# Performance work log

Measured on AMD Instinct MI355X. Metric: run time of the kernel, lower is better.

The kernel has to match this reference:

```python
import jax, jax.numpy as jnp
import numpy as np

N = 65536      # nodes
E = 1048576    # edges (avg in-degree ~16)
C = 128        # in_channels = out_channels = edge_dim
T = 4          # towers
F_IN = C // T  # 32 (divide_input=True)
F_OUT = C // T # 32

# degree histogram from the repo: degrees 1..6 with these counts
_counts = np.array([108477, 299931, 180702, 10767, 3, 2], dtype=np.float64)
_degs = np.arange(1, 7, dtype=np.float64)
AVG_LIN = float((_counts * _degs).sum() / _counts.sum())
AVG_LOG = float((_counts * np.log(_degs + 1.0)).sum() / _counts.sum())


def setup_inputs() -> dict:
    key = jax.random.key(0)
    ks = jax.random.split(key, 8)
    def w(k, shape, fan_in):
        return (jax.random.normal(k, shape, jnp.float32) / np.sqrt(fan_in)).astype(jnp.float32)
    return {
        "x": jax.random.normal(ks[0], (N, C), jnp.float32),
        "edge_attr": jax.random.normal(ks[1], (E, C), jnp.float32),
        "edge_index": jax.random.randint(ks[2], (2, E), 0, N, jnp.int32),
        "W_edge": w(ks[3], (F_IN, C), C),
        "b_edge": jnp.zeros((F_IN,), jnp.float32),
        "W_pre": w(ks[4], (T, 3 * F_IN, F_IN), 3 * F_IN),
        "b_pre": jnp.zeros((T, F_IN), jnp.float32),
        "W_post": w(ks[5], (T, 13 * F_IN, F_OUT), 13 * F_IN),
        "b_post": jnp.zeros((T, F_OUT), jnp.float32),
        "W_lin": w(ks[6], (C, C), C),
        "b_lin": jnp.zeros((C,), jnp.float32),
    }


def reference(x, edge_attr, edge_index, W_edge, b_edge, W_pre, b_pre, W_post, b_post, W_lin, b_lin):
    src, dst = edge_index[0], edge_index[1]  # PyG: messages from src (x_j) aggregated at dst (x_i)
    xt = x.reshape(N, T, F_IN)               # divide_input=True: split channels across towers

    # edge encoder, broadcast across towers
    e = edge_attr @ W_edge.T + b_edge        # [E, F_in]
    e = jnp.broadcast_to(e[:, None, :], (E, T, F_IN))

    # message: gather + concat + per-tower pretrans Linear
    h = jnp.concatenate([xt[dst], xt[src], e], axis=-1)      # [E, T, 3F]
    m = jnp.einsum('etf,tfg->etg', h, W_pre) + b_pre          # [E, T, F]

    # multi-aggregator scatter-reduce over destination nodes
    cnt = jax.ops.segment_sum(jnp.ones((E,), m.dtype), dst, N)    # in-degree [N]
    cnt_safe = jnp.maximum(cnt, 1.0)[:, None, None]
    msum = jax.ops.segment_sum(m, dst, N)
    mean = msum / cnt_safe
    mean_sq = jax.ops.segment_sum(m * m, dst, N) / cnt_safe
    std = jnp.sqrt(jax.nn.relu(mean_sq - mean * mean) + 1e-5)
    empty = (cnt == 0)[:, None, None]
    mx = jnp.where(empty, 0.0, jax.ops.segment_max(m, dst, N))
    mn = jnp.where(empty, 0.0, jax.ops.segment_min(m, dst, N))
    agg = jnp.concatenate([mean, mx, mn, std], axis=-1)       # [N, T, 4F]

    # degree scalers: identity, amplification, attenuation
    deg = cnt[:, None, None]
    logd = jnp.log(deg + 1.0)
    amp = agg * (logd / AVG_LOG)
    att = agg * jnp.where(deg == 0, 1.0, AVG_LOG / jnp.where(deg == 0, 1.0, logd))
    out = jnp.concatenate([agg, amp, att], axis=-1)           # [N, T, 12F]

    # posttrans: concat self features, per-tower Linear, merge towers
    out = jnp.concatenate([xt, out], axis=-1)                 # [N, T, 13F]
    out = jnp.einsum('ntf,tfg->ntg', out, W_post) + b_post    # [N, T, F_out]
    out = out.reshape(N, C)
    return out @ W_lin.T + b_lin + x  # residual
```

## Files before the change

kernel.cpp:

```cpp
#include <hip/hip_runtime.h>
#include <math.h>

__global__ __launch_bounds__(256) void pre_kernel(
    const float* __restrict__ x, const float* __restrict__ W_pre,
    float* __restrict__ ps)
{
  __shared__ float xl[2][128];
  const int tid = threadIdx.x;
  const int nl  = tid >> 7;
  const int j   = tid & 127;
  const int n   = blockIdx.x * 2 + nl;
  xl[nl][j] = x[(size_t)n * 128 + j];
  __syncthreads();
  const int t = j >> 5, g = j & 31;
  const float* xp = &xl[nl][t * 32];
  const float* Ws = W_pre + (size_t)(t * 96 + 32) * 32 + g;
  float aps = 0.f;
#pragma unroll
  for (int f = 0; f < 32; ++f) aps += xp[f] * Ws[f * 32];
  ps[(size_t)n * 128 + j] = aps;
}

__global__ __launch_bounds__(256) void count_kernel(
    const int* __restrict__ ei, int* __restrict__ cnt, int E)
{
  const int e = blockIdx.x * 256 + threadIdx.x;
  if (e < E) atomicAdd(&cnt[ei[E + e]], 1);
}

__global__ __launch_bounds__(256) void scan_kernel(
    const int* __restrict__ cnt, int* __restrict__ base, int* __restrict__ fill)
{
  __shared__ int part[256];
  const int tid = threadIdx.x;
  const int c0 = tid * 256;
  int s = 0;
  for (int i = 0; i < 256; ++i) s += cnt[c0 + i];
  part[tid] = s;
  __syncthreads();
  if (tid == 0) {
    int run = 0;
    for (int i = 0; i < 256; ++i) { int t = part[i]; part[i] = run; run += t; }
  }
  __syncthreads();
  int run = part[tid];
  for (int i = 0; i < 256; ++i) {
    int cc = cnt[c0 + i];
    base[c0 + i] = run;
    fill[c0 + i] = run;
    run += cc;
  }
}

__global__ __launch_bounds__(256) void scatter_kernel(
    const int* __restrict__ ei, int* __restrict__ fill,
    int* __restrict__ eid_s, int* __restrict__ srcs_s, int E)
{
  const int e = blockIdx.x * 256 + threadIdx.x;
  if (e < E) {
    const int d = ei[E + e];
    const int slot = atomicAdd(&fill[d], 1);
    eid_s[slot] = e;
    srcs_s[slot] = ei[e];
  }
}

__global__ __launch_bounds__(256) void agg_kernel(
    const float* __restrict__ x, const float* __restrict__ edge_attr,
    const float* __restrict__ W_edge, const float* __restrict__ b_edge,
    const float* __restrict__ W_pre, const float* __restrict__ b_pre,
    const float* __restrict__ ps, const int* __restrict__ eid_s,
    const int* __restrict__ srcs_s, const int* __restrict__ cnt,
    const int* __restrict__ base, float* __restrict__ aggs)
{
  __shared__ float sEA[4][128];
  __shared__ float sE[4][32];
  __shared__ float sX[4][128];
  const int tid  = threadIdx.x;
  const int lane = tid & 63;
  const int w    = tid >> 6;
  const int g    = lane & 31;
  const int half = lane >> 5;
  const int t0   = half;
  const int n    = blockIdx.x * 4 + w;

  float we[64];
  {
    const float4* wrow = (const float4*)(W_edge + (size_t)g * 128 + half * 64);
#pragma unroll
    for (int k = 0; k < 16; ++k) {
      const float4 q = wrow[k];
      we[4*k] = q.x; we[4*k+1] = q.y; we[4*k+2] = q.z; we[4*k+3] = q.w;
    }
  }
  float wp0[32], wp1[32];
#pragma unroll
  for (int f = 0; f < 32; ++f) {
    wp0[f] = W_pre[(size_t)(t0 * 96 + 64 + f) * 32 + g];
    wp1[f] = W_pre[(size_t)((t0 + 2) * 96 + 64 + f) * 32 + g];
  }
  const float bedge = b_edge[g];

  sX[w][lane]      = x[(size_t)n * 128 + lane];
  sX[w][lane + 64] = x[(size_t)n * 128 + 64 + lane];
  float pd0 = b_pre[t0 * 32 + g];
  float pd1 = b_pre[(t0 + 2) * 32 + g];
#pragma unroll
  for (int f = 0; f < 32; ++f) {
    pd0 += sX[w][t0 * 32 + f]       * W_pre[(size_t)(t0 * 96 + f) * 32 + g];
    pd1 += sX[w][(t0 + 2) * 32 + f] * W_pre[(size_t)((t0 + 2) * 96 + f) * 32 + g];
  }

  const int c  = cnt[n];
  const int b0 = base[n];
  float sum0 = 0.f, sum1 = 0.f, sq0 = 0.f, sq1 = 0.f;
  float mx0 = -INFINITY, mx1 = -INFINITY, mn0 = INFINITY, mn1 = INFINITY;
  for (int i = 0; i < c; ++i) {
    const int idx = b0 + i;
    const int eid = eid_s[idx];
    const int s   = srcs_s[idx];
    const float2 v = *(const float2*)(edge_attr + (size_t)eid * 128 + lane * 2);
    *(float2*)&sEA[w][lane * 2] = v;
    const float ps0 = ps[(size_t)s * 128 + lane];
    const float ps1 = ps[(size_t)s * 128 + 64 + lane];
    float acc = 0.f;
    const float4* eap = (const float4*)&sEA[w][half * 64];
#pragma unroll
    for (int k = 0; k < 16; ++k) {
      const float4 q = eap[k];
      acc += q.x * we[4*k] + q.y * we[4*k+1] + q.z * we[4*k+2] + q.w * we[4*k+3];
    }
    acc += __shfl_xor(acc, 32);
    sE[w][g] = acc + bedge;
    float a0 = 0.f, a1 = 0.f;
    const float4* ep = (const float4*)sE[w];
#pragma unroll
    for (int k = 0; k < 8; ++k) {
      const float4 q = ep[k];
      a0 += q.x * wp0[4*k] + q.y * wp0[4*k+1] + q.z * wp0[4*k+2] + q.w * wp0[4*k+3];
      a1 += q.x * wp1[4*k] + q.y * wp1[4*k+1] + q.z * wp1[4*k+2] + q.w * wp1[4*k+3];
    }
    const float m0 = a0 + pd0 + ps0;
    const float m1 = a1 + pd1 + ps1;
    sum0 += m0; sq0 += m0 * m0; mx0 = fmaxf(mx0, m0); mn0 = fminf(mn0, m0);
    sum1 += m1; sq1 += m1 * m1; mx1 = fmaxf(mx1, m1); mn1 = fminf(mn1, m1);
  }

  const float csafe = fmaxf((float)c, 1.f);
  const float mean0 = sum0 / csafe, mean1 = sum1 / csafe;
  const float sd0 = sqrtf(fmaxf(sq0 / csafe - mean0 * mean0, 0.f) + 1e-5f);
  const float sd1 = sqrtf(fmaxf(sq1 / csafe - mean1 * mean1, 0.f) + 1e-5f);
  if (c == 0) { mx0 = mx1 = mn0 = mn1 = 0.f; }
  float* ag = aggs + (size_t)n * 512;
  ag[lane]       = mean0; ag[64 + lane]  = mean1;
  ag[128 + lane] = mx0;   ag[192 + lane] = mx1;
  ag[256 + lane] = mn0;   ag[320 + lane] = mn1;
  ag[384 + lane] = sd0;   ag[448 + lane] = sd1;
}

__global__ __launch_bounds__(256) void post_kernel(
    const float* __restrict__ x, const float* __restrict__ aggs,
    const int* __restrict__ cnt,
    const float* __restrict__ W_post, const float* __restrict__ b_post,
    const float* __restrict__ W_lin, const float* __restrict__ b_lin,
    float* __restrict__ out, float avg_log)
{
  __shared__ float vec[8][4][416];
  __shared__ float h2[8][128];
  const int tid = threadIdx.x;
  const int j = tid & 127;
  const int t = j >> 5, g = j & 31;
  const int n0 = blockIdx.x * 8;

  for (int itn = 0; itn < 4; ++itn) {
    const int nl = itn * 2 + (tid >> 7);
    const int n = n0 + nl;
    const size_t o = (size_t)n * 128 + j;
    const float* ag = aggs + (size_t)n * 512;
    const float c = (float)cnt[n];
    const float mean = ag[j];
    const float mx   = ag[128 + j];
    const float mn   = ag[256 + j];
    const float sd   = ag[384 + j];
    const float logd = logf(c + 1.f);
    const float amp_s = logd / avg_log;
    const float att_s = (c == 0.f) ? 1.f : (avg_log / logd);
    float* v = vec[nl][t];
    v[g]        = x[o];
    v[32 + g]   = mean;          v[64 + g]   = mx;
    v[96 + g]   = mn;            v[128 + g]  = sd;
    v[160 + g]  = mean * amp_s;  v[192 + g]  = mx * amp_s;
    v[224 + g]  = mn * amp_s;    v[256 + g]  = sd * amp_s;
    v[288 + g]  = mean * att_s;  v[320 + g]  = mx * att_s;
    v[352 + g]  = mn * att_s;    v[384 + g]  = sd * att_s;
  }
  __syncthreads();

  {
    const int nlb = tid >> 7;
    const float b = b_post[t * 32 + g];
    float acc0 = b, acc1 = b, acc2 = b, acc3 = b;
    const float* Wp = W_post + (size_t)(t * 416) * 32 + g;
    const float* v0 = vec[nlb + 0][t];
    const float* v1 = vec[nlb + 2][t];
    const float* v2 = vec[nlb + 4][t];
    const float* v3 = vec[nlb + 6][t];
    for (int f = 0; f < 416; ++f) {
      const float wv = Wp[(size_t)f * 32];
      acc0 += v0[f] * wv; acc1 += v1[f] * wv;
      acc2 += v2[f] * wv; acc3 += v3[f] * wv;
    }
    h2[nlb + 0][j] = acc0; h2[nlb + 2][j] = acc1;
    h2[nlb + 4][j] = acc2; h2[nlb + 6][j] = acc3;
  }
  __syncthreads();

  {
    const int nlb = tid >> 7;
    const float* Wl = W_lin + (size_t)j * 128;
    const float bl = b_lin[j];
    float a0 = bl, a1 = bl, a2 = bl, a3 = bl;
    const float* h0 = h2[nlb + 0];
    const float* h1 = h2[nlb + 2];
    const float* hp = h2[nlb + 4];
    const float* h3 = h2[nlb + 6];
    for (int k = 0; k < 128; ++k) {
      const float wv = Wl[k];
      a0 += h0[k] * wv; a1 += h1[k] * wv;
      a2 += hp[k] * wv; a3 += h3[k] * wv;
    }
    const size_t b0 = (size_t)(n0 + nlb + 0) * 128 + j;
    const size_t b1 = (size_t)(n0 + nlb + 2) * 128 + j;
    const size_t b2 = (size_t)(n0 + nlb + 4) * 128 + j;
    const size_t b3 = (size_t)(n0 + nlb + 6) * 128 + j;
    out[b0] = a0 + x[b0];
    out[b1] = a1 + x[b1];
    out[b2] = a2 + x[b2];
    out[b3] = a3 + x[b3];
  }
}

extern "C" void kernel_launch(void* const* d_in, const int* in_sizes, int n_in,
                              void* d_out, int out_size, void* d_ws, size_t ws_size,
                              hipStream_t stream) {
  const float* x         = (const float*)d_in[0];
  const float* edge_attr = (const float*)d_in[1];
  const int*   ei        = (const int*)  d_in[2];
  const float* W_edge    = (const float*)d_in[3];
  const float* b_edge    = (const float*)d_in[4];
  const float* W_pre     = (const float*)d_in[5];
  const float* b_pre     = (const float*)d_in[6];
  const float* W_post    = (const float*)d_in[7];
  const float* b_post    = (const float*)d_in[8];
  const float* W_lin     = (const float*)d_in[9];
  const float* b_lin     = (const float*)d_in[10];
  float* out = (float*)d_out;

  const int N = in_sizes[0] / 128;
  const int E = in_sizes[2] / 2;

  float* ps    = (float*)d_ws;
  float* aggs  = ps + (size_t)N * 128;
  int*   eid_s = (int*)(aggs + (size_t)N * 512);
  int*   srcs_s = eid_s + E;
  int*   cnt   = srcs_s + E;
  int*   base  = cnt + N;
  int*   fill  = base + N;

  hipMemsetAsync(cnt, 0, (size_t)N * 4, stream);

  const double counts[6] = {108477.0, 299931.0, 180702.0, 10767.0, 3.0, 2.0};
  double num = 0.0, den = 0.0;
  for (int i = 0; i < 6; ++i) { num += counts[i] * log((double)(i + 2)); den += counts[i]; }
  const float avg_log = (float)(num / den);

  pre_kernel<<<N / 2, 256, 0, stream>>>(x, W_pre, ps);
  count_kernel<<<(E + 255) / 256, 256, 0, stream>>>(ei, cnt, E);
  scan_kernel<<<1, 256, 0, stream>>>(cnt, base, fill);
  scatter_kernel<<<(E + 255) / 256, 256, 0, stream>>>(ei, fill, eid_s, srcs_s, E);
  agg_kernel<<<N / 4, 256, 0, stream>>>(x, edge_attr, W_edge, b_edge, W_pre, b_pre,
                                        ps, eid_s, srcs_s, cnt, base, aggs);
  post_kernel<<<N / 8, 256, 0, stream>>>(x, aggs, cnt, W_post, b_post,
                                         W_lin, b_lin, out, avg_log);
}
```

Measured before the change: 2.018 ms.

## Move edge encoder into scatter pass and prefetch sorted edge features in aggregation

```diff
diff --git a/kernel.cpp b/kernel.cpp
--- a/kernel.cpp
+++ b/kernel.cpp
@@ -52,29 +52,74 @@
   }
 }
 
-__global__ __launch_bounds__(256) void scatter_kernel(
-    const int* __restrict__ ei, int* __restrict__ fill,
-    int* __restrict__ eid_s, int* __restrict__ srcs_s, int E)
-{
-  const int e = blockIdx.x * 256 + threadIdx.x;
-  if (e < E) {
+__global__ __launch_bounds__(256) void escatter_kernel(
+    const float* __restrict__ edge_attr, const int* __restrict__ ei,
+    const float* __restrict__ W_edge, const float* __restrict__ b_edge,
+    int* __restrict__ fill, int* __restrict__ srcs_s,
+    float* __restrict__ e_sorted, int E)
+{
+  __shared__ float sEA[4][2][128];
+  const int tid  = threadIdx.x;
+  const int lane = tid & 63;
+  const int w    = tid >> 6;
+  const int g    = lane & 31;
+  const int half = lane >> 5;
+  const int e4   = (blockIdx.x * 4 + w) * 4;
+  if (e4 >= E) return;
+  const int nv = min(4, E - e4);
+
+  float we[64];
+  {
+    const float4* wrow = (const float4*)(W_edge + (size_t)g * 128 + half * 64);
+#pragma unroll
+    for (int k = 0; k < 16; ++k) {
+      const float4 q = wrow[k];
+      we[4*k] = q.x; we[4*k+1] = q.y; we[4*k+2] = q.z; we[4*k+3] = q.w;
+    }
+  }
+  const float bedge = b_edge[g];
+
+  int slot = 0;
+  if (lane < nv) {
+    const int e = e4 + lane;
     const int d = ei[E + e];
-    const int slot = atomicAdd(&fill[d], 1);
-    eid_s[slot] = e;
-    srcs_s[slot] = ei[e];
+    const int s = ei[e];
+    slot = atomicAdd(&fill[d], 1);
+    srcs_s[slot] = s;
+  }
+
+  float2 va[4];
+#pragma unroll
+  for (int l = 0; l < 4; ++l) {
+    const int el = (l < nv) ? (e4 + l) : e4;
+    va[l] = *(const float2*)(edge_attr + (size_t)el * 128 + lane * 2);
+  }
+
+#pragma unroll
+  for (int l = 0; l < 4; ++l) {
+    if (l >= nv) break;
+    *(float2*)&sEA[w][l & 1][lane * 2] = va[l];
+    float acc = 0.f;
+    const float4* eap = (const float4*)&sEA[w][l & 1][half * 64];
+#pragma unroll
+    for (int k = 0; k < 16; ++k) {
+      const float4 q = eap[k];
+      acc += q.x * we[4*k] + q.y * we[4*k+1] + q.z * we[4*k+2] + q.w * we[4*k+3];
+    }
+    acc += __shfl_xor(acc, 32);
+    const int sl = __shfl(slot, l);
+    if (half == 0) e_sorted[(size_t)sl * 32 + g] = acc + bedge;
   }
 }
 
 __global__ __launch_bounds__(256) void agg_kernel(
-    const float* __restrict__ x, const float* __restrict__ edge_attr,
-    const float* __restrict__ W_edge, const float* __restrict__ b_edge,
+    const float* __restrict__ x,
     const float* __restrict__ W_pre, const float* __restrict__ b_pre,
-    const float* __restrict__ ps, const int* __restrict__ eid_s,
+    const float* __restrict__ ps, const float* __restrict__ e_sorted,
     const int* __restrict__ srcs_s, const int* __restrict__ cnt,
     const int* __restrict__ base, float* __restrict__ aggs)
 {
-  __shared__ float sEA[4][128];
-  __shared__ float sE[4][32];
+  __shared__ float sE[4][2][64];
   __shared__ float sX[4][128];
   const int tid  = threadIdx.x;
   const int lane = tid & 63;
@@ -84,22 +129,12 @@
   const int t0   = half;
   const int n    = blockIdx.x * 4 + w;
 
-  float we[64];
-  {
-    const float4* wrow = (const float4*)(W_edge + (size_t)g * 128 + half * 64);
-#pragma unroll
-    for (int k = 0; k < 16; ++k) {
-      const float4 q = wrow[k];
-      we[4*k] = q.x; we[4*k+1] = q.y; we[4*k+2] = q.z; we[4*k+3] = q.w;
-    }
-  }
   float wp0[32], wp1[32];
 #pragma unroll
   for (int f = 0; f < 32; ++f) {
     wp0[f] = W_pre[(size_t)(t0 * 96 + 64 + f) * 32 + g];
     wp1[f] = W_pre[(size_t)((t0 + 2) * 96 + 64 + f) * 32 + g];
   }
-  const float bedge = b_edge[g];
 
   sX[w][lane]      = x[(size_t)n * 128 + lane];
   sX[w][lane + 64] = x[(size_t)n * 128 + 64 + lane];
@@ -115,35 +150,61 @@
   const int b0 = base[n];
   float sum0 = 0.f, sum1 = 0.f, sq0 = 0.f, sq1 = 0.f;
   float mx0 = -INFINITY, mx1 = -INFINITY, mn0 = INFINITY, mn1 = INFINITY;
-  for (int i = 0; i < c; ++i) {
-    const int idx = b0 + i;
-    const int eid = eid_s[idx];
-    const int s   = srcs_s[idx];
-    const float2 v = *(const float2*)(edge_attr + (size_t)eid * 128 + lane * 2);
-    *(float2*)&sEA[w][lane * 2] = v;
-    const float ps0 = ps[(size_t)s * 128 + lane];
-    const float ps1 = ps[(size_t)s * 128 + 64 + lane];
-    float acc = 0.f;
-    const float4* eap = (const float4*)&sEA[w][half * 64];
-#pragma unroll
-    for (int k = 0; k < 16; ++k) {
-      const float4 q = eap[k];
-      acc += q.x * we[4*k] + q.y * we[4*k+1] + q.z * we[4*k+2] + q.w * we[4*k+3];
-    }
-    acc += __shfl_xor(acc, 32);
-    sE[w][g] = acc + bedge;
-    float a0 = 0.f, a1 = 0.f;
-    const float4* ep = (const float4*)sE[w];
-#pragma unroll
-    for (int k = 0; k < 8; ++k) {
-      const float4 q = ep[k];
-      a0 += q.x * wp0[4*k] + q.y * wp0[4*k+1] + q.z * wp0[4*k+2] + q.w * wp0[4*k+3];
-      a1 += q.x * wp1[4*k] + q.y * wp1[4*k+1] + q.z * wp1[4*k+2] + q.w * wp1[4*k+3];
-    }
-    const float m0 = a0 + pd0 + ps0;
-    const float m1 = a1 + pd1 + ps1;
-    sum0 += m0; sq0 += m0 * m0; mx0 = fmaxf(mx0, m0); mn0 = fminf(mn0, m0);
-    sum1 += m1; sq1 += m1 * m1; mx1 = fmaxf(mx1, m1); mn1 = fminf(mn1, m1);
+
+  float ev = 0.f, pA0 = 0.f, pA1 = 0.f, pB0 = 0.f, pB1 = 0.f;
+  if (c > 0) {
+    const int cm = c - 1;
+    ev = e_sorted[(size_t)(b0 + min(half, cm)) * 32 + g];
+    const int sA = srcs_s[b0];
+    const int sB = srcs_s[b0 + min(1, cm)];
+    pA0 = ps[(size_t)sA * 128 + lane];
+    pA1 = ps[(size_t)sA * 128 + 64 + lane];
+    pB0 = ps[(size_t)sB * 128 + lane];
+    pB1 = ps[(size_t)sB * 128 + 64 + lane];
+  }
+
+  for (int i = 0; i < c; i += 2) {
+    const int buf = (i >> 1) & 1;
+    const int cm  = c - 1;
+    const float ev_n = e_sorted[(size_t)(b0 + min(i + 2 + half, cm)) * 32 + g];
+    const int sAn = srcs_s[b0 + min(i + 2, cm)];
+    const int sBn = srcs_s[b0 + min(i + 3, cm)];
+    const float pA0n = ps[(size_t)sAn * 128 + lane];
+    const float pA1n = ps[(size_t)sAn * 128 + 64 + lane];
+    const float pB0n = ps[(size_t)sBn * 128 + lane];
+    const float pB1n = ps[(size_t)sBn * 128 + 64 + lane];
+
+    sE[w][buf][lane] = ev;
+
+    {
+      float a0 = 0.f, a1 = 0.f;
+      const float4* ep = (const float4*)&sE[w][buf][0];
+#pragma unroll
+      for (int k = 0; k < 8; ++k) {
+        const float4 q = ep[k];
+        a0 += q.x * wp0[4*k] + q.y * wp0[4*k+1] + q.z * wp0[4*k+2] + q.w * wp0[4*k+3];
+        a1 += q.x * wp1[4*k] + q.y * wp1[4*k+1] + q.z * wp1[4*k+2] + q.w * wp1[4*k+3];
+      }
+      const float m0 = a0 + pd0 + pA0;
+      const float m1 = a1 + pd1 + pA1;
+      sum0 += m0; sq0 += m0 * m0; mx0 = fmaxf(mx0, m0); mn0 = fminf(mn0, m0);
+      sum1 += m1; sq1 += m1 * m1; mx1 = fmaxf(mx1, m1); mn1 = fminf(mn1, m1);
+    }
+    if (i + 1 < c) {
+      float a0 = 0.f, a1 = 0.f;
+      const float4* ep = (const float4*)&sE[w][buf][32];
+#pragma unroll
+      for (int k = 0; k < 8; ++k) {
+        const float4 q = ep[k];
+        a0 += q.x * wp0[4*k] + q.y * wp0[4*k+1] + q.z * wp0[4*k+2] + q.w * wp0[4*k+3];
+        a1 += q.x * wp1[4*k] + q.y * wp1[4*k+1] + q.z * wp1[4*k+2] + q.w * wp1[4*k+3];
+      }
+      const float m0 = a0 + pd0 + pB0;
+      const float m1 = a1 + pd1 + pB1;
+      sum0 += m0; sq0 += m0 * m0; mx0 = fmaxf(mx0, m0); mn0 = fminf(mn0, m0);
+      sum1 += m1; sq1 += m1 * m1; mx1 = fmaxf(mx1, m1); mn1 = fminf(mn1, m1);
+    }
+    ev = ev_n; pA0 = pA0n; pA1 = pA1n; pB0 = pB0n; pB1 = pB1n;
   }
 
   const float csafe = fmaxf((float)c, 1.f);
@@ -259,13 +320,13 @@
   const int N = in_sizes[0] / 128;
   const int E = in_sizes[2] / 2;
 
-  float* ps    = (float*)d_ws;
-  float* aggs  = ps + (size_t)N * 128;
-  int*   eid_s = (int*)(aggs + (size_t)N * 512);
-  int*   srcs_s = eid_s + E;
-  int*   cnt   = srcs_s + E;
-  int*   base  = cnt + N;
-  int*   fill  = base + N;
+  float* ps       = (float*)d_ws;
+  float* aggs     = ps + (size_t)N * 128;
+  float* e_sorted = aggs + (size_t)N * 512;
+  int*   srcs_s   = (int*)(e_sorted + (size_t)E * 32);
+  int*   cnt      = srcs_s + E;
+  int*   base     = cnt + N;
+  int*   fill     = base + N;
 
   hipMemsetAsync(cnt, 0, (size_t)N * 4, stream);
 
@@ -277,9 +338,10 @@
   pre_kernel<<<N / 2, 256, 0, stream>>>(x, W_pre, ps);
   count_kernel<<<(E + 255) / 256, 256, 0, stream>>>(ei, cnt, E);
   scan_kernel<<<1, 256, 0, stream>>>(cnt, base, fill);
-  scatter_kernel<<<(E + 255) / 256, 256, 0, stream>>>(ei, fill, eid_s, srcs_s, E);
-  agg_kernel<<<N / 4, 256, 0, stream>>>(x, edge_attr, W_edge, b_edge, W_pre, b_pre,
-                                        ps, eid_s, srcs_s, cnt, base, aggs);
+  escatter_kernel<<<(E + 15) / 16, 256, 0, stream>>>(edge_attr, ei, W_edge, b_edge,
+                                                     fill, srcs_s, e_sorted, E);
+  agg_kernel<<<N / 4, 256, 0, stream>>>(x, W_pre, b_pre, ps, e_sorted,
+                                        srcs_s, cnt, base, aggs);
   post_kernel<<<N / 8, 256, 0, stream>>>(x, aggs, cnt, W_post, b_post,
                                          W_lin, b_lin, out, avg_log);
 }
```

After: 1.846 ms. 8.5% less time.
